# Performance work log

Hardware: AMD Instinct MI355X
Metric: run time of the kernel (lower is better)

Reference implementation:

```python
import jax, jax.numpy as jnp
import numpy as np

B, C, H, W = 8, 64, 160, 160
N_HEADS = 8
EPS = 1e-6


def conv1x1(x, w, b):
    # x: [B, Cin, H, W], w: [Cout, Cin], b: [Cout]
    return jnp.einsum('oc,bchw->bohw', w, x) + b[None, :, None, None]


def setup_inputs() -> dict:
    key = jax.random.key(0)
    ks = jax.random.split(key, 12)
    s = 0.05
    return {
        'high': jax.random.normal(ks[0], (B, C, H, W), jnp.float32),
        'low': jax.random.normal(ks[1], (B, C, H, W), jnp.float32),
        'wq_high': jax.random.normal(ks[2], (C // 2, C), jnp.float32) * s,
        'bq_high': jnp.zeros((C // 2,), jnp.float32),
        'wq_low': jax.random.normal(ks[3], (C // 2, C), jnp.float32) * s,
        'bq_low': jnp.zeros((C // 2,), jnp.float32),
        'wk': jax.random.normal(ks[4], (C, C), jnp.float32) * s,
        'bk': jnp.zeros((C,), jnp.float32),
        'wv': jax.random.normal(ks[5], (C, C), jnp.float32) * s,
        'bv': jnp.zeros((C,), jnp.float32),
        'wo': jax.random.normal(ks[6], (C, C), jnp.float32) * s,
        'bo': jnp.zeros((C,), jnp.float32),
    }


def reference(high, low, wq_high, bq_high, wq_low, bq_low, wk, bk, wv, bv, wo, bo):
    b, c, h, w = low.shape
    p, d, n = N_HEADS, c // N_HEADS, h * w
    # q branches: [B, C//2, H, W] -> [B, P/2, N, d]
    hq = conv1x1(high, wq_high, bq_high).reshape(b, p // 2, d, n).transpose(0, 1, 3, 2)
    lq = conv1x1(low, wq_low, bq_low).reshape(b, p // 2, d, n).transpose(0, 1, 3, 2)
    q = jax.nn.softplus(jnp.concatenate([hq, lq], axis=1))          # [B, P, N, d]
    k = jax.nn.softplus(conv1x1(low, wk, bk).reshape(b, p, d, n))   # [B, P, d, N]
    v = conv1x1(low, wv, bv).reshape(b, p, d, n)                    # [B, P, d, N]
    # linear-attention context: kT v over spatial N
    attn_map = jnp.einsum('bpmn,bpcn->bpmc', k, v)                  # [B, P, d, d]
    norm = 1.0 / jnp.einsum('bpnc,bpc->bpn', q, jnp.sum(k, axis=-1) + EPS)  # [B, P, N]
    out = jnp.einsum('bpnm,bpmc,bpn->bpcn', q, attn_map, norm)      # [B, P, d, N]
    out = out.reshape(b, c, h, w)
    return conv1x1(out, wo, bo)
```

## Files before the change

### kernel.cpp

```cpp
#include <hip/hip_runtime.h>

#define NPIX  25600
#define NB    8
#define NCH   200
#define KPX   128
#define EPSV  1e-6f

#define WS_WQM   0
#define WS_BQM   4096
#define WS_WKVM  4160
#define WS_BKVM  12352
#define WS_KSE   12480
#define WS_PART  12992
#define WS_GM    934592

typedef __attribute__((ext_vector_type(8))) short short8v;
typedef __attribute__((ext_vector_type(4))) float f32x4v;

__device__ __forceinline__ unsigned short f2bf(float x) {
  unsigned u = __float_as_uint(x);
  return (unsigned short)((u + 0x7FFFu + ((u >> 16) & 1u)) >> 16);
}
__device__ __forceinline__ float bf2f(unsigned short h) {
  return __uint_as_float(((unsigned)h) << 16);
}
__device__ __forceinline__ float softplus_(float x) {
  return (x > 20.0f) ? x : __logf(1.0f + __expf(x));
}

__global__ void k0_pack(const float* __restrict__ wq_high, const float* __restrict__ bq_high,
                        const float* __restrict__ wq_low,  const float* __restrict__ bq_low,
                        const float* __restrict__ wk, const float* __restrict__ bk,
                        const float* __restrict__ wv, const float* __restrict__ bv,
                        float* __restrict__ ws) {
  const int tid = threadIdx.x;
  unsigned short* wqm = (unsigned short*)(ws + WS_WQM);
  for (int e = tid; e < 8192; e += 256) {
    int j = e & 7, l = (e >> 3) & 63, frag = e >> 9;
    int sp = frag & 1, ks = (frag >> 1) & 1, mt = frag >> 2;
    int row = mt * 16 + (l & 15), c = ks * 32 + (l >> 4) * 8 + j;
    int head = row >> 3, m = row & 7;
    float v = (head < 4) ? wq_high[(head * 8 + m) * 64 + c]
                         : wq_low[((head - 4) * 8 + m) * 64 + c];
    unsigned short hb = f2bf(v);
    wqm[e] = (sp == 0) ? hb : f2bf(v - bf2f(hb));
  }
  for (int e = tid; e < 64; e += 256) {
    int head = e >> 3, m = e & 7;
    ws[WS_BQM + e] = (head < 4) ? bq_high[head * 8 + m] : bq_low[(head - 4) * 8 + m];
  }
  unsigned short* wmp = (unsigned short*)(ws + WS_WKVM);
  for (int e = tid; e < 16384; e += 256) {
    int j = e & 7, l = (e >> 3) & 63, frag = e >> 9;
    int sp = frag & 1, ks = (frag >> 1) & 1, mt = frag >> 2;
    int row = l & 15, k32 = (l >> 4) * 8 + j, c = ks * 32 + k32;
    int head = (mt & 3) * 2 + (row >> 3), m = row & 7;
    float wv_ = (mt < 4) ? wk[(head * 8 + m) * 64 + c] : wv[(head * 8 + m) * 64 + c];
    unsigned short hb = f2bf(wv_);
    wmp[e] = (sp == 0) ? hb : f2bf(wv_ - bf2f(hb));
  }
  for (int e = tid; e < 128; e += 256) {
    int mt = e >> 4, row = e & 15;
    int head = (mt & 3) * 2 + (row >> 3), m = row & 7;
    ws[WS_BKVM + e] = (mt < 4) ? bk[head * 8 + m] : bv[head * 8 + m];
  }
}

__global__ __attribute__((amdgpu_waves_per_eu(1, 8)))
void k1_kv(const float* __restrict__ low,
           const float* __restrict__ ws,
           float* __restrict__ part) {
  const int b = blockIdx.y, chunk = blockIdx.x;
  const int tid = threadIdx.x, lane = tid & 63;
  const int w = __builtin_amdgcn_readfirstlane(tid >> 6);
  const int l15 = lane & 15, lg = lane >> 4;
  __shared__ float kvL[16384];
  const float* lowb = low + (size_t)b * 64 * NPIX + chunk * KPX;
  short8v xhi[2], xlo[2];
#pragma unroll
  for (int ks = 0; ks < 2; ks++) {
    const float* xp = lowb + (size_t)(ks * 32 + lg * 8) * NPIX + w * 16 + l15;
    float xs[8];
#pragma unroll
    for (int j = 0; j < 8; j++) xs[j] = xp[(size_t)j * NPIX];
#pragma unroll
    for (int j = 0; j < 8; j++) {
      unsigned short h = f2bf(xs[j]);
      xhi[ks][j] = (short)h;
      xlo[ks][j] = (short)f2bf(xs[j] - bf2f(h));
    }
  }
  const unsigned short* wm = (const unsigned short*)(ws + WS_WKVM);
  const float* bm = ws + WS_BKVM;
#pragma unroll
  for (int mt = 0; mt < 8; mt++) {
    f32x4v a0 = {0.f, 0.f, 0.f, 0.f};
#pragma unroll
    for (int ks = 0; ks < 2; ks++) {
      short8v whi = *(const short8v*)(wm + (((mt * 4 + ks * 2 + 0) * 64) + lane) * 8);
      short8v wlo = *(const short8v*)(wm + (((mt * 4 + ks * 2 + 1) * 64) + lane) * 8);
      a0 = __builtin_amdgcn_mfma_f32_16x16x32_bf16(whi, xhi[ks], a0, 0, 0, 0);
      a0 = __builtin_amdgcn_mfma_f32_16x16x32_bf16(whi, xlo[ks], a0, 0, 0, 0);
      a0 = __builtin_amdgcn_mfma_f32_16x16x32_bf16(wlo, xhi[ks], a0, 0, 0, 0);
    }
#pragma unroll
    for (int r = 0; r < 4; r++) {
      const int row = mt * 16 + lg * 4 + r;
      float v0 = a0[r] + bm[row];
      if (mt < 4) v0 = softplus_(v0);
      const int px = w * 16 + l15;
      kvL[row * 128 + ((((px >> 2) ^ (row & 7))) << 2) + (px & 3)] = v0;
    }
  }
  __syncthreads();
  const int col = l15;
  const int h = w;
  f32x4v acc = {0.f, 0.f, 0.f, 0.f};
  const int arow = h * 8 + (l15 & 7);
  const int brow = 64 + h * 8 + (col < 8 ? col : 0);
#pragma unroll
  for (int ks = 0; ks < 4; ks++) {
    const int pxl = ks * 32 + lg * 8;
    const int sA = arow & 7;
    float4 af0 = *(const float4*)&kvL[arow * 128 + (((pxl >> 2) ^ sA) << 2)];
    float4 af1 = *(const float4*)&kvL[arow * 128 + ((((pxl >> 2) + 1) ^ sA) << 2)];
    float as[8] = {af0.x, af0.y, af0.z, af0.w, af1.x, af1.y, af1.z, af1.w};
    float bs[8];
    if (col < 8) {
      const int sB = brow & 7;
      float4 bf0 = *(const float4*)&kvL[brow * 128 + (((pxl >> 2) ^ sB) << 2)];
      float4 bf1 = *(const float4*)&kvL[brow * 128 + ((((pxl >> 2) + 1) ^ sB) << 2)];
      bs[0]=bf0.x; bs[1]=bf0.y; bs[2]=bf0.z; bs[3]=bf0.w;
      bs[4]=bf1.x; bs[5]=bf1.y; bs[6]=bf1.z; bs[7]=bf1.w;
    } else {
      const float fill = (col == 8) ? 1.0f : 0.0f;
#pragma unroll
      for (int j = 0; j < 8; j++) bs[j] = fill;
    }
    short8v ahi, alo, bhi, blo;
#pragma unroll
    for (int j = 0; j < 8; j++) {
      unsigned short ha = f2bf(as[j]);
      ahi[j] = (short)ha; alo[j] = (short)f2bf(as[j] - bf2f(ha));
      unsigned short hb = f2bf(bs[j]);
      bhi[j] = (short)hb; blo[j] = (short)f2bf(bs[j] - bf2f(hb));
    }
    acc = __builtin_amdgcn_mfma_f32_16x16x32_bf16(ahi, bhi, acc, 0, 0, 0);
    acc = __builtin_amdgcn_mfma_f32_16x16x32_bf16(ahi, blo, acc, 0, 0, 0);
    acc = __builtin_amdgcn_mfma_f32_16x16x32_bf16(alo, bhi, acc, 0, 0, 0);
  }
  if (lane < 32 && col <= 8) {
    float* pb = part + ((size_t)(b * 8 + h) * NCH + chunk) * 72;
#pragma unroll
    for (int r = 0; r < 4; r++) {
      const int rr = lg * 4 + r;
      if (col < 8) pb[rr * 8 + col] = acc[r];
      else         pb[64 + rr] = acc[r];
    }
  }
}

__global__ void k2_g(const float* __restrict__ part, const float* __restrict__ wo,
                     float* __restrict__ ws) {
  const int b = blockIdx.x >> 3, p = blockIdx.x & 7;
  const int tid = threadIdx.x, lane = tid & 63, sub = tid >> 6;
  __shared__ float red[4][72];
  __shared__ float attnL[72];
  const float* src = part + (size_t)(b * 8 + p) * NCH * 72;
  float s0 = 0.0f, s1 = 0.0f;
  for (int ch = sub * (NCH / 4); ch < (sub + 1) * (NCH / 4); ch++) {
    s0 += src[ch * 72 + lane];
    if (lane < 8) s1 += src[ch * 72 + 64 + lane];
  }
  red[sub][lane] = s0;
  if (lane < 8) red[sub][64 + lane] = s1;
  __syncthreads();
  if (tid < 72) attnL[tid] = (red[0][tid] + red[1][tid]) + (red[2][tid] + red[3][tid]);
  __syncthreads();
  if (tid >= 64) {
    if (tid < 72) ws[WS_KSE + (b * 8 + p) * 8 + (tid - 64)] = attnL[tid] + EPSV;
    return;
  }
  const int o = tid;
  float wrow[8];
#pragma unroll
  for (int c = 0; c < 8; c++) wrow[c] = wo[o * 64 + p * 8 + c];
  unsigned short* gm = (unsigned short*)(ws + WS_GM) + (size_t)b * 8192;
  const int mt2 = o >> 4, lane_ = (p & 3) * 16 + (o & 15), ks = p >> 2;
  short8v hi8, lo8;
#pragma unroll
  for (int m = 0; m < 8; m++) {
    float g = 0.0f;
#pragma unroll
    for (int c = 0; c < 8; c++) g = fmaf(attnL[m * 8 + c], wrow[c], g);
    unsigned short hb = f2bf(g);
    hi8[m] = (short)hb;
    lo8[m] = (short)f2bf(g - bf2f(hb));
  }
  *(short8v*)(gm + (size_t)((mt2 * 4 + ks * 2 + 0) * 64 + lane_) * 8) = hi8;
  *(short8v*)(gm + (size_t)((mt2 * 4 + ks * 2 + 1) * 64 + lane_) * 8) = lo8;
}

__global__ __attribute__((amdgpu_waves_per_eu(1, 8)))
void k3_main(const float* __restrict__ high,
             const float* __restrict__ low,
             const float* __restrict__ ws,
             const float* __restrict__ bo,
             float* __restrict__ out) {
  const int b = blockIdx.y, chunk = blockIdx.x;
  const int tid = threadIdx.x, lane = tid & 63;
  const int w = __builtin_amdgcn_readfirstlane(tid >> 6);
  const int l15 = lane & 15, lg = lane >> 4;
  __shared__ float qL[8192];
  __shared__ float rnL[1024];
  const float* highb = high + (size_t)b * 64 * NPIX + chunk * KPX;
  const float* lowb  = low  + (size_t)b * 64 * NPIX + chunk * KPX;
  short8v xhi[2][2], xlo[2][2];
#pragma unroll
  for (int s = 0; s < 2; s++) {
    const float* srcb = (s == 0) ? highb : lowb;
#pragma unroll
    for (int ks = 0; ks < 2; ks++) {
      const float* xp = srcb + (size_t)(ks * 32 + lg * 8) * NPIX + w * 16 + l15;
      float xs[8];
#pragma unroll
      for (int j = 0; j < 8; j++) xs[j] = xp[(size_t)j * NPIX];
#pragma unroll
      for (int j = 0; j < 8; j++) {
        unsigned short h = f2bf(xs[j]);
        xhi[s][ks][j] = (short)h;
        xlo[s][ks][j] = (short)f2bf(xs[j] - bf2f(h));
      }
    }
  }
  const unsigned short* wqm = (const unsigned short*)(ws + WS_WQM);
  const float* bqm = ws + WS_BQM;
#pragma unroll
  for (int mt = 0; mt < 4; mt++) {
    const int s = mt >> 1;
    f32x4v a0 = {0.f, 0.f, 0.f, 0.f};
#pragma unroll
    for (int ks = 0; ks < 2; ks++) {
      short8v whi = *(const short8v*)(wqm + (((mt * 4 + ks * 2 + 0) * 64) + lane) * 8);
      short8v wlo = *(const short8v*)(wqm + (((mt * 4 + ks * 2 + 1) * 64) + lane) * 8);
      a0 = __builtin_amdgcn_mfma_f32_16x16x32_bf16(whi, xhi[s][ks], a0, 0, 0, 0);
      a0 = __builtin_amdgcn_mfma_f32_16x16x32_bf16(whi, xlo[s][ks], a0, 0, 0, 0);
      a0 = __builtin_amdgcn_mfma_f32_16x16x32_bf16(wlo, xhi[s][ks], a0, 0, 0, 0);
    }
#pragma unroll
    for (int r = 0; r < 4; r++) {
      const int row = mt * 16 + lg * 4 + r;
      float v0 = softplus_(a0[r] + bqm[row]);
      const int px = w * 16 + l15;
      qL[row * 128 + ((((px >> 2) ^ (row & 7))) << 2) + (px & 3)] = v0;
    }
  }
  __syncthreads();
  {
    const int px = tid & 127;
#pragma unroll
    for (int h0 = 0; h0 < 2; h0++) {
      const int h = (tid >> 7) * 2 + h0;
      const float* ksep = ws + WS_KSE + (b * 8 + h) * 8;
      float s = 0.0f;
#pragma unroll
      for (int m = 0; m < 8; m++) {
        const int row = h * 8 + m;
        s = fmaf(qL[row * 128 + ((((px >> 2) ^ (row & 7))) << 2) + (px & 3)],
                 ksep[m], s);
      }
      rnL[h * 128 + px] = 1.0f / s;
    }
  }
  __syncthreads();
  const unsigned short* gm = (const unsigned short*)(ws + WS_GM) + (size_t)b * 8192;
  const int px = w * 16 + l15;
  short8v qhi[2], qlo[2];
#pragma unroll
  for (int ks = 0; ks < 2; ks++) {
    const float rn = rnL[(ks * 4 + lg) * 128 + px];
#pragma unroll
    for (int j = 0; j < 8; j++) {
      const int row = ks * 32 + lg * 8 + j;
      float q = qL[row * 128 + ((((px >> 2) ^ j)) << 2) + (px & 3)] * rn;
      unsigned short h = f2bf(q);
      qhi[ks][j] = (short)h;
      qlo[ks][j] = (short)f2bf(q - bf2f(h));
    }
  }
  f32x4v acc[4];
#pragma unroll
  for (int mt2 = 0; mt2 < 4; mt2++) acc[mt2] = (f32x4v){0.f, 0.f, 0.f, 0.f};
#pragma unroll
  for (int mt2 = 0; mt2 < 4; mt2++) {
#pragma unroll
    for (int ks = 0; ks < 2; ks++) {
      short8v ghi = *(const short8v*)(gm + (size_t)((mt2 * 4 + ks * 2 + 0) * 64 + lane) * 8);
      short8v glo = *(const short8v*)(gm + (size_t)((mt2 * 4 + ks * 2 + 1) * 64 + lane) * 8);
      acc[mt2] = __builtin_amdgcn_mfma_f32_16x16x32_bf16(ghi, qhi[ks], acc[mt2], 0, 0, 0);
      acc[mt2] = __builtin_amdgcn_mfma_f32_16x16x32_bf16(ghi, qlo[ks], acc[mt2], 0, 0, 0);
      acc[mt2] = __builtin_amdgcn_mfma_f32_16x16x32_bf16(glo, qhi[ks], acc[mt2], 0, 0, 0);
    }
  }
  float* ob = out + ((size_t)b * 64) * NPIX + chunk * KPX + px;
#pragma unroll
  for (int mt2 = 0; mt2 < 4; mt2++)
#pragma unroll
    for (int r = 0; r < 4; r++) {
      const int o = mt2 * 16 + lg * 4 + r;
      ob[(size_t)o * NPIX] = acc[mt2][r] + bo[o];
    }
}

extern "C" void kernel_launch(void* const* d_in, const int* in_sizes, int n_in,
                              void* d_out, int out_size, void* d_ws, size_t ws_size,
                              hipStream_t stream) {
  const float* high    = (const float*)d_in[0];
  const float* low     = (const float*)d_in[1];
  const float* wq_high = (const float*)d_in[2];
  const float* bq_high = (const float*)d_in[3];
  const float* wq_low  = (const float*)d_in[4];
  const float* bq_low  = (const float*)d_in[5];
  const float* wk      = (const float*)d_in[6];
  const float* bk      = (const float*)d_in[7];
  const float* wv      = (const float*)d_in[8];
  const float* bv      = (const float*)d_in[9];
  const float* wo      = (const float*)d_in[10];
  const float* bo      = (const float*)d_in[11];
  float* ws  = (float*)d_ws;
  float* out = (float*)d_out;

  k0_pack<<<1, 256, 0, stream>>>(wq_high, bq_high, wq_low, bq_low, wk, bk, wv, bv, ws);
  dim3 grid(NCH, NB);
  k1_kv<<<grid, 512, 0, stream>>>(low, ws, ws + WS_PART);
  k2_g<<<64, 256, 0, stream>>>(ws + WS_PART, wo, ws);
  k3_main<<<grid, 512, 0, stream>>>(high, low, ws, bo, out);
}
```

Before: 113.6 us.

## Switch split-precision MFMA from bf16 to fp16 and store k/v pre-split in LDS

Replaces the bf16 hi/lo split with an fp16 hi/lo split throughout, using hardware casts instead of manual rounding bit-tricks, and switches all MFMAs to the f16 variant. In the kv kernel, k/v values are now split into fp16 hi/lo once at write time and kept in two half-precision LDS planes, so the reduction stage loads ready-made fragments instead of reloading floats and re-splitting them per iteration. The normalized q is scaled by 4096 before splitting to avoid fp16 underflow, and the output is rescaled afterward. Fp16's narrower exponent range could overflow or underflow for other input scales.

```diff
diff --git a/kernel.cpp b/kernel.cpp
--- a/kernel.cpp
+++ b/kernel.cpp
@@ -14,15 +14,12 @@
 #define WS_PART  12992
 #define WS_GM    934592
 
-typedef __attribute__((ext_vector_type(8))) short short8v;
+typedef __attribute__((ext_vector_type(8))) _Float16 half8v;
 typedef __attribute__((ext_vector_type(4))) float f32x4v;
 
-__device__ __forceinline__ unsigned short f2bf(float x) {
-  unsigned u = __float_as_uint(x);
-  return (unsigned short)((u + 0x7FFFu + ((u >> 16) & 1u)) >> 16);
-}
-__device__ __forceinline__ float bf2f(unsigned short h) {
-  return __uint_as_float(((unsigned)h) << 16);
+__device__ __forceinline__ void split_h(float x, _Float16& hi, _Float16& lo) {
+  hi = (_Float16)x;
+  lo = (_Float16)(x - (float)hi);
 }
 __device__ __forceinline__ float softplus_(float x) {
   return (x > 20.0f) ? x : __logf(1.0f + __expf(x));
@@ -34,7 +31,7 @@
                         const float* __restrict__ wv, const float* __restrict__ bv,
                         float* __restrict__ ws) {
   const int tid = threadIdx.x;
-  unsigned short* wqm = (unsigned short*)(ws + WS_WQM);
+  _Float16* wqm = (_Float16*)(ws + WS_WQM);
   for (int e = tid; e < 8192; e += 256) {
     int j = e & 7, l = (e >> 3) & 63, frag = e >> 9;
     int sp = frag & 1, ks = (frag >> 1) & 1, mt = frag >> 2;
@@ -42,22 +39,22 @@
     int head = row >> 3, m = row & 7;
     float v = (head < 4) ? wq_high[(head * 8 + m) * 64 + c]
                          : wq_low[((head - 4) * 8 + m) * 64 + c];
-    unsigned short hb = f2bf(v);
-    wqm[e] = (sp == 0) ? hb : f2bf(v - bf2f(hb));
+    _Float16 hi, lo; split_h(v, hi, lo);
+    wqm[e] = (sp == 0) ? hi : lo;
   }
   for (int e = tid; e < 64; e += 256) {
     int head = e >> 3, m = e & 7;
     ws[WS_BQM + e] = (head < 4) ? bq_high[head * 8 + m] : bq_low[(head - 4) * 8 + m];
   }
-  unsigned short* wmp = (unsigned short*)(ws + WS_WKVM);
+  _Float16* wmp = (_Float16*)(ws + WS_WKVM);
   for (int e = tid; e < 16384; e += 256) {
     int j = e & 7, l = (e >> 3) & 63, frag = e >> 9;
     int sp = frag & 1, ks = (frag >> 1) & 1, mt = frag >> 2;
     int row = l & 15, k32 = (l >> 4) * 8 + j, c = ks * 32 + k32;
     int head = (mt & 3) * 2 + (row >> 3), m = row & 7;
     float wv_ = (mt < 4) ? wk[(head * 8 + m) * 64 + c] : wv[(head * 8 + m) * 64 + c];
-    unsigned short hb = f2bf(wv_);
-    wmp[e] = (sp == 0) ? hb : f2bf(wv_ - bf2f(hb));
+    _Float16 hi, lo; split_h(wv_, hi, lo);
+    wmp[e] = (sp == 0) ? hi : lo;
   }
   for (int e = tid; e < 128; e += 256) {
     int mt = e >> 4, row = e & 15;
@@ -74,9 +71,9 @@
   const int tid = threadIdx.x, lane = tid & 63;
   const int w = __builtin_amdgcn_readfirstlane(tid >> 6);
   const int l15 = lane & 15, lg = lane >> 4;
-  __shared__ float kvL[16384];
+  __shared__ _Float16 kvP[2][16384];
   const float* lowb = low + (size_t)b * 64 * NPIX + chunk * KPX;
-  short8v xhi[2], xlo[2];
+  half8v xhi[2], xlo[2];
 #pragma unroll
   for (int ks = 0; ks < 2; ks++) {
     const float* xp = lowb + (size_t)(ks * 32 + lg * 8) * NPIX + w * 16 + l15;
@@ -84,24 +81,20 @@
 #pragma unroll
     for (int j = 0; j < 8; j++) xs[j] = xp[(size_t)j * NPIX];
 #pragma unroll
-    for (int j = 0; j < 8; j++) {
-      unsigned short h = f2bf(xs[j]);
-      xhi[ks][j] = (short)h;
-      xlo[ks][j] = (short)f2bf(xs[j] - bf2f(h));
-    }
-  }
-  const unsigned short* wm = (const unsigned short*)(ws + WS_WKVM);
+    for (int j = 0; j < 8; j++) { _Float16 h, l; split_h(xs[j], h, l); xhi[ks][j] = h; xlo[ks][j] = l; }
+  }
+  const _Float16* wm = (const _Float16*)(ws + WS_WKVM);
   const float* bm = ws + WS_BKVM;
 #pragma unroll
   for (int mt = 0; mt < 8; mt++) {
     f32x4v a0 = {0.f, 0.f, 0.f, 0.f};
 #pragma unroll
     for (int ks = 0; ks < 2; ks++) {
-      short8v whi = *(const short8v*)(wm + (((mt * 4 + ks * 2 + 0) * 64) + lane) * 8);
-      short8v wlo = *(const short8v*)(wm + (((mt * 4 + ks * 2 + 1) * 64) + lane) * 8);
-      a0 = __builtin_amdgcn_mfma_f32_16x16x32_bf16(whi, xhi[ks], a0, 0, 0, 0);
-      a0 = __builtin_amdgcn_mfma_f32_16x16x32_bf16(whi, xlo[ks], a0, 0, 0, 0);
-      a0 = __builtin_amdgcn_mfma_f32_16x16x32_bf16(wlo, xhi[ks], a0, 0, 0, 0);
+      half8v whi = *(const half8v*)(wm + (((mt * 4 + ks * 2 + 0) * 64) + lane) * 8);
+      half8v wlo = *(const half8v*)(wm + (((mt * 4 + ks * 2 + 1) * 64) + lane) * 8);
+      a0 = __builtin_amdgcn_mfma_f32_16x16x32_f16(whi, xhi[ks], a0, 0, 0, 0);
+      a0 = __builtin_amdgcn_mfma_f32_16x16x32_f16(whi, xlo[ks], a0, 0, 0, 0);
+      a0 = __builtin_amdgcn_mfma_f32_16x16x32_f16(wlo, xhi[ks], a0, 0, 0, 0);
     }
 #pragma unroll
     for (int r = 0; r < 4; r++) {
@@ -109,7 +102,10 @@
       float v0 = a0[r] + bm[row];
       if (mt < 4) v0 = softplus_(v0);
       const int px = w * 16 + l15;
-      kvL[row * 128 + ((((px >> 2) ^ (row & 7))) << 2) + (px & 3)] = v0;
+      const int idx = row * 128 + ((((px >> 3) ^ (row & 7)) << 3) | (px & 7));
+      _Float16 hi, lo; split_h(v0, hi, lo);
+      kvP[0][idx] = hi;
+      kvP[1][idx] = lo;
     }
   }
   __syncthreads();
@@ -120,34 +116,20 @@
   const int brow = 64 + h * 8 + (col < 8 ? col : 0);
 #pragma unroll
   for (int ks = 0; ks < 4; ks++) {
-    const int pxl = ks * 32 + lg * 8;
-    const int sA = arow & 7;
-    float4 af0 = *(const float4*)&kvL[arow * 128 + (((pxl >> 2) ^ sA) << 2)];
-    float4 af1 = *(const float4*)&kvL[arow * 128 + ((((pxl >> 2) + 1) ^ sA) << 2)];
-    float as[8] = {af0.x, af0.y, af0.z, af0.w, af1.x, af1.y, af1.z, af1.w};
-    float bs[8];
-    if (col < 8) {
-      const int sB = brow & 7;
-      float4 bf0 = *(const float4*)&kvL[brow * 128 + (((pxl >> 2) ^ sB) << 2)];
-      float4 bf1 = *(const float4*)&kvL[brow * 128 + ((((pxl >> 2) + 1) ^ sB) << 2)];
-      bs[0]=bf0.x; bs[1]=bf0.y; bs[2]=bf0.z; bs[3]=bf0.w;
-      bs[4]=bf1.x; bs[5]=bf1.y; bs[6]=bf1.z; bs[7]=bf1.w;
-    } else {
-      const float fill = (col == 8) ? 1.0f : 0.0f;
-#pragma unroll
-      for (int j = 0; j < 8; j++) bs[j] = fill;
-    }
-    short8v ahi, alo, bhi, blo;
-#pragma unroll
-    for (int j = 0; j < 8; j++) {
-      unsigned short ha = f2bf(as[j]);
-      ahi[j] = (short)ha; alo[j] = (short)f2bf(as[j] - bf2f(ha));
-      unsigned short hb = f2bf(bs[j]);
-      bhi[j] = (short)hb; blo[j] = (short)f2bf(bs[j] - bf2f(hb));
-    }
-    acc = __builtin_amdgcn_mfma_f32_16x16x32_bf16(ahi, bhi, acc, 0, 0, 0);
-    acc = __builtin_amdgcn_mfma_f32_16x16x32_bf16(ahi, blo, acc, 0, 0, 0);
-    acc = __builtin_amdgcn_mfma_f32_16x16x32_bf16(alo, bhi, acc, 0, 0, 0);
+    const int unitA = (((ks * 4 + lg) ^ (arow & 7)) << 3);
+    const int unitB = (((ks * 4 + lg) ^ (brow & 7)) << 3);
+    half8v ahi = *(const half8v*)&kvP[0][arow * 128 + unitA];
+    half8v alo = *(const half8v*)&kvP[1][arow * 128 + unitA];
+    half8v bhi = *(const half8v*)&kvP[0][brow * 128 + unitB];
+    half8v blo = *(const half8v*)&kvP[1][brow * 128 + unitB];
+    if (col >= 8) {
+      const _Float16 fh = (col == 8) ? (_Float16)1.0f : (_Float16)0.0f;
+#pragma unroll
+      for (int j = 0; j < 8; j++) { bhi[j] = fh; blo[j] = (_Float16)0.0f; }
+    }
+    acc = __builtin_amdgcn_mfma_f32_16x16x32_f16(ahi, bhi, acc, 0, 0, 0);
+    acc = __builtin_amdgcn_mfma_f32_16x16x32_f16(ahi, blo, acc, 0, 0, 0);
+    acc = __builtin_amdgcn_mfma_f32_16x16x32_f16(alo, bhi, acc, 0, 0, 0);
   }
   if (lane < 32 && col <= 8) {
     float* pb = part + ((size_t)(b * 8 + h) * NCH + chunk) * 72;
@@ -185,20 +167,19 @@
   float wrow[8];
 #pragma unroll
   for (int c = 0; c < 8; c++) wrow[c] = wo[o * 64 + p * 8 + c];
-  unsigned short* gm = (unsigned short*)(ws + WS_GM) + (size_t)b * 8192;
+  _Float16* gm = (_Float16*)(ws + WS_GM) + (size_t)b * 8192;
   const int mt2 = o >> 4, lane_ = (p & 3) * 16 + (o & 15), ks = p >> 2;
-  short8v hi8, lo8;
+  half8v hi8, lo8;
 #pragma unroll
   for (int m = 0; m < 8; m++) {
     float g = 0.0f;
 #pragma unroll
     for (int c = 0; c < 8; c++) g = fmaf(attnL[m * 8 + c], wrow[c], g);
-    unsigned short hb = f2bf(g);
-    hi8[m] = (short)hb;
-    lo8[m] = (short)f2bf(g - bf2f(hb));
-  }
-  *(short8v*)(gm + (size_t)((mt2 * 4 + ks * 2 + 0) * 64 + lane_) * 8) = hi8;
-  *(short8v*)(gm + (size_t)((mt2 * 4 + ks * 2 + 1) * 64 + lane_) * 8) = lo8;
+    _Float16 hi, lo; split_h(g, hi, lo);
+    hi8[m] = hi; lo8[m] = lo;
+  }
+  *(half8v*)(gm + (size_t)((mt2 * 4 + ks * 2 + 0) * 64 + lane_) * 8) = hi8;
+  *(half8v*)(gm + (size_t)((mt2 * 4 + ks * 2 + 1) * 64 + lane_) * 8) = lo8;
 }
 
 __global__ __attribute__((amdgpu_waves_per_eu(1, 8)))
@@ -215,7 +196,7 @@
   __shared__ float rnL[1024];
   const float* highb = high + (size_t)b * 64 * NPIX + chunk * KPX;
   const float* lowb  = low  + (size_t)b * 64 * NPIX + chunk * KPX;
-  short8v xhi[2][2], xlo[2][2];
+  half8v xhi[2][2], xlo[2][2];
 #pragma unroll
   for (int s = 0; s < 2; s++) {
     const float* srcb = (s == 0) ? highb : lowb;
@@ -226,14 +207,10 @@
 #pragma unroll
       for (int j = 0; j < 8; j++) xs[j] = xp[(size_t)j * NPIX];
 #pragma unroll
-      for (int j = 0; j < 8; j++) {
-        unsigned short h = f2bf(xs[j]);
-        xhi[s][ks][j] = (short)h;
-        xlo[s][ks][j] = (short)f2bf(xs[j] - bf2f(h));
-      }
-    }
-  }
-  const unsigned short* wqm = (const unsigned short*)(ws + WS_WQM);
+      for (int j = 0; j < 8; j++) { _Float16 h, l; split_h(xs[j], h, l); xhi[s][ks][j] = h; xlo[s][ks][j] = l; }
+    }
+  }
+  const _Float16* wqm = (const _Float16*)(ws + WS_WQM);
   const float* bqm = ws + WS_BQM;
 #pragma unroll
   for (int mt = 0; mt < 4; mt++) {
@@ -241,11 +218,11 @@
     f32x4v a0 = {0.f, 0.f, 0.f, 0.f};
 #pragma unroll
     for (int ks = 0; ks < 2; ks++) {
-      short8v whi = *(const short8v*)(wqm + (((mt * 4 + ks * 2 + 0) * 64) + lane) * 8);
-      short8v wlo = *(const short8v*)(wqm + (((mt * 4 + ks * 2 + 1) * 64) + lane) * 8);
-      a0 = __builtin_amdgcn_mfma_f32_16x16x32_bf16(whi, xhi[s][ks], a0, 0, 0, 0);
-      a0 = __builtin_amdgcn_mfma_f32_16x16x32_bf16(whi, xlo[s][ks], a0, 0, 0, 0);
-      a0 = __builtin_amdgcn_mfma_f32_16x16x32_bf16(wlo, xhi[s][ks], a0, 0, 0, 0);
+      half8v whi = *(const half8v*)(wqm + (((mt * 4 + ks * 2 + 0) * 64) + lane) * 8);
+      half8v wlo = *(const half8v*)(wqm + (((mt * 4 + ks * 2 + 1) * 64) + lane) * 8);
+      a0 = __builtin_amdgcn_mfma_f32_16x16x32_f16(whi, xhi[s][ks], a0, 0, 0, 0);
+      a0 = __builtin_amdgcn_mfma_f32_16x16x32_f16(whi, xlo[s][ks], a0, 0, 0, 0);
+      a0 = __builtin_amdgcn_mfma_f32_16x16x32_f16(wlo, xhi[s][ks], a0, 0, 0, 0);
     }
 #pragma unroll
     for (int r = 0; r < 4; r++) {
@@ -273,19 +250,18 @@
     }
   }
   __syncthreads();
-  const unsigned short* gm = (const unsigned short*)(ws + WS_GM) + (size_t)b * 8192;
+  const _Float16* gm = (const _Float16*)(ws + WS_GM) + (size_t)b * 8192;
   const int px = w * 16 + l15;
-  short8v qhi[2], qlo[2];
+  half8v qhi[2], qlo[2];
 #pragma unroll
   for (int ks = 0; ks < 2; ks++) {
-    const float rn = rnL[(ks * 4 + lg) * 128 + px];
+    const float rn4k = rnL[(ks * 4 + lg) * 128 + px] * 4096.0f;
 #pragma unroll
     for (int j = 0; j < 8; j++) {
       const int row = ks * 32 + lg * 8 + j;
-      float q = qL[row * 128 + ((((px >> 2) ^ j)) << 2) + (px & 3)] * rn;
-      unsigned short h = f2bf(q);
-      qhi[ks][j] = (short)h;
-      qlo[ks][j] = (short)f2bf(q - bf2f(h));
+      float q = qL[row * 128 + ((((px >> 2) ^ j)) << 2) + (px & 3)] * rn4k;
+      _Float16 h, l; split_h(q, h, l);
+      qhi[ks][j] = h; qlo[ks][j] = l;
     }
   }
   f32x4v acc[4];
@@ -295,11 +271,11 @@
   for (int mt2 = 0; mt2 < 4; mt2++) {
 #pragma unroll
     for (int ks = 0; ks < 2; ks++) {
-      short8v ghi = *(const short8v*)(gm + (size_t)((mt2 * 4 + ks * 2 + 0) * 64 + lane) * 8);
-      short8v glo = *(const short8v*)(gm + (size_t)((mt2 * 4 + ks * 2 + 1) * 64 + lane) * 8);
-      acc[mt2] = __builtin_amdgcn_mfma_f32_16x16x32_bf16(ghi, qhi[ks], acc[mt2], 0, 0, 0);
-      acc[mt2] = __builtin_amdgcn_mfma_f32_16x16x32_bf16(ghi, qlo[ks], acc[mt2], 0, 0, 0);
-      acc[mt2] = __builtin_amdgcn_mfma_f32_16x16x32_bf16(glo, qhi[ks], acc[mt2], 0, 0, 0);
+      half8v ghi = *(const half8v*)(gm + (size_t)((mt2 * 4 + ks * 2 + 0) * 64 + lane) * 8);
+      half8v glo = *(const half8v*)(gm + (size_t)((mt2 * 4 + ks * 2 + 1) * 64 + lane) * 8);
+      acc[mt2] = __builtin_amdgcn_mfma_f32_16x16x32_f16(ghi, qhi[ks], acc[mt2], 0, 0, 0);
+      acc[mt2] = __builtin_amdgcn_mfma_f32_16x16x32_f16(ghi, qlo[ks], acc[mt2], 0, 0, 0);
+      acc[mt2] = __builtin_amdgcn_mfma_f32_16x16x32_f16(glo, qhi[ks], acc[mt2], 0, 0, 0);
     }
   }
   float* ob = out + ((size_t)b * 64) * NPIX + chunk * KPX + px;
@@ -308,7 +284,7 @@
 #pragma unroll
     for (int r = 0; r < 4; r++) {
       const int o = mt2 * 16 + lg * 4 + r;
-      ob[(size_t)o * NPIX] = acc[mt2][r] + bo[o];
+      ob[(size_t)o * NPIX] = acc[mt2][r] * 0.000244140625f + bo[o];
     }
 }
 
```

Result: faster. 106.6 us (-6.1%).
